# Kernel tuning notes

Hardware: AMD Instinct MI355X
Metric: run time of the kernel (lower is better)

## Reference

```python
import jax, jax.numpy as jnp
import numpy as np

N, T, IN_F, H, C_OUT, R = 50000, 128, 6, 32, 32, 16
NUM_EDGES, N_INC = 2000, 150000


def setup_inputs() -> dict:
    key = jax.random.key(0)
    ks = jax.random.split(key, 16)
    s = 0.1  # param scale
    return {
        "price_input": jax.random.normal(ks[0], (N, T, IN_F), jnp.float32),
        "concept": jax.random.normal(ks[1], (N_INC,), jnp.float32),
        "W_ih": jax.random.normal(ks[2], (3 * H, IN_F), jnp.float32) * s,
        "W_hh": jax.random.normal(ks[3], (3 * H, H), jnp.float32) * s,
        "b_ih": jax.random.normal(ks[4], (3 * H,), jnp.float32) * s,
        "b_hh": jax.random.normal(ks[5], (3 * H,), jnp.float32) * s,
        "W1": jax.random.normal(ks[6], (C_OUT, H), jnp.float32) * s,
        "b1": jax.random.normal(ks[7], (C_OUT,), jnp.float32) * s,
        "W2": jax.random.normal(ks[8], (H, C_OUT), jnp.float32) * s,
        "b2": jax.random.normal(ks[9], (H,), jnp.float32) * s,
        "Wl": jax.random.normal(ks[10], (R, H), jnp.float32) * s,
        "bl": jax.random.normal(ks[11], (R,), jnp.float32) * s,
        "node_idx": jax.random.randint(ks[12], (N_INC,), 0, N, dtype=jnp.int32),
        "edge_idx": jax.random.randint(ks[13], (N_INC,), 0, NUM_EDGES, dtype=jnp.int32),
    }


def gru_last_hidden(x, W_ih, W_hh, b_ih, b_hh):
    # x: [N, T, IN_F] -> final hidden state [N, H] (PyTorch GRU, gate order r,z,n)
    gi_all = jnp.einsum('nti,gi->tng', x, W_ih) + b_ih  # [T, N, 3H]
    h0 = jnp.zeros((x.shape[0], W_hh.shape[1]), x.dtype)

    def step(h, gi):
        gh = h @ W_hh.T + b_hh
        ir, iz, i_n = jnp.split(gi, 3, axis=-1)
        hr, hz, h_n = jnp.split(gh, 3, axis=-1)
        r = jax.nn.sigmoid(ir + hr)
        z = jax.nn.sigmoid(iz + hz)
        n = jnp.tanh(i_n + r * h_n)
        return (1.0 - z) * n + z * h, None

    hT, _ = jax.lax.scan(step, h0, gi_all)
    return hT


def hypergraph_conv(x, W, b, node_idx, edge_idx, num_nodes, num_edges):
    # PyG HypergraphConv, use_attention=False, hyperedge_weight=1:
    # out = D^{-1} H B^{-1} H^T (X W^T) + b
    xw = x @ W.T  # [N, F_out]
    ones = jnp.ones(node_idx.shape[0], x.dtype)
    B = jax.ops.segment_sum(ones, edge_idx, num_segments=num_edges)
    Binv = jnp.where(B > 0, 1.0 / B, 0.0)
    edge_feat = jax.ops.segment_sum(xw[node_idx], edge_idx, num_segments=num_edges)
    edge_feat = edge_feat * Binv[:, None]
    D = jax.ops.segment_sum(ones, node_idx, num_segments=num_nodes)
    Dinv = jnp.where(D > 0, 1.0 / D, 0.0)
    out = jax.ops.segment_sum(edge_feat[edge_idx], node_idx, num_segments=num_nodes)
    return out * Dinv[:, None] + b


def reference(price_input, concept, W_ih, W_hh, b_ih, b_hh, W1, b1, W2, b2, Wl, bl, node_idx, edge_idx):
    # concept is only consumed on the PreAttn path (disabled here), kept for signature parity.
    num_nodes = price_input.shape[0]
    output = gru_last_hidden(price_input, W_ih, W_hh, b_ih, b_hh)  # query[0] -> [N, c_in]
    output = jax.nn.leaky_relu(output, 0.01)
    x = jax.nn.leaky_relu(
        hypergraph_conv(output, W1, b1, node_idx, edge_idx, num_nodes, NUM_EDGES), 0.2)
    x = jax.nn.leaky_relu(
        hypergraph_conv(x, W2, b2, node_idx, edge_idx, num_nodes, NUM_EDGES), 0.2)
    return jax.nn.leaky_relu(x @ Wl.T + bl, 0.01)  # [N, len(rr_num)]
```

## Files before the change

### kernel.cpp

```cpp
#include <hip/hip_runtime.h>
#include <hip/hip_bf16.h>
#include <cstdint>

#define NN 50000
#define TT 128
#define INF 6
#define HH 32
#define NE 2000
#define NI 150000
#define RR 16

typedef __attribute__((ext_vector_type(4)))  float f32x4;
typedef __attribute__((ext_vector_type(16))) float f32x16;
typedef __attribute__((ext_vector_type(8)))  short short8;

__device__ __forceinline__ float lrelu(float x, float s){ return x > 0.f ? x : s*x; }

__device__ __forceinline__ unsigned pk2(float a, float b){
  union { __hip_bfloat162 h; unsigned u; } t;
  t.h = __float22bfloat162_rn(make_float2(a, b));
  return t.u;
}
__device__ __forceinline__ void pkhl(float a, float b, unsigned &hi, unsigned &lo){
  hi = pk2(a, b);
  float ha = __uint_as_float(hi << 16);
  float hb = __uint_as_float(hi & 0xFFFF0000u);
  lo = pk2(a - ha, b - hb);
}
__device__ __forceinline__ unsigned pksplit(float x){
  unsigned h = pk2(x, 0.f) & 0xFFFFu;
  float hf = __uint_as_float(h << 16);
  unsigned l = pk2(x - hf, 0.f) & 0xFFFFu;
  return h | (l << 16);
}
__device__ __forceinline__ short8 mk8(unsigned a, unsigned b, unsigned c, unsigned d){
  union { unsigned u[4]; short8 v; } t;
  t.u[0]=a; t.u[1]=b; t.u[2]=c; t.u[3]=d;
  return t.v;
}
#define MFMA32 __builtin_amdgcn_mfma_f32_32x32x16_bf16

__global__ __launch_bounds__(64,2) void gru_mfma(
    const float* __restrict__ price,
    const float* __restrict__ W_ih, const float* __restrict__ W_hh,
    const float* __restrict__ b_ih, const float* __restrict__ b_hh,
    const float* __restrict__ W1,
    float* __restrict__ xw, float* __restrict__ eaccZ)
{
  __shared__ __align__(16) unsigned xs[2][2048];

  const int lane = threadIdx.x;
  const int a    = lane & 31;
  const int hb   = lane >> 5;
  const int n0   = blockIdx.x*32;

  { int gt = blockIdx.x*64 + lane; if (gt < NE*HH) eaccZ[gt] = 0.f; }

  for (int idx = lane; idx < 512; idx += 64){
    int bsel = idx >> 8, rem = idx & 255;
    int nd = rem >> 3, t7 = rem & 7;
    int swz = (nd&7)<<2;
    xs[bsel][nd*64 + ((t7*8+6) ^ swz)] = 0x3F803F80u;
    xs[bsel][nd*64 + ((t7*8+7) ^ swz)] = 0u;
  }

  short8 AxA[3], Ahh[3][2], Ahl[3][2];
#pragma unroll
  for (int T=0; T<3; T++){
    const int gr = T*32 + a;
    const float sc = (T<2) ? -1.44269504f : 2.88539008f;
    const float* vi = W_ih + gr*INF;
    const float w0=vi[0]*sc, w1=vi[1]*sc, w2=vi[2]*sc, w3=vi[3]*sc, w4=vi[4]*sc, w5=vi[5]*sc;
    const float bias = (b_ih[gr] + ((T<2) ? b_hh[gr] : 0.f)) * sc;
    if (hb==0) AxA[T] = mk8(pk2(w0,w1), pk2(w2,w3), pk2(w4,w5), pk2(w0,w1));
    else       AxA[T] = mk8(pk2(w2,w3), pk2(w4,w5), pksplit(bias), 0u);
#pragma unroll
    for (int m=0; m<2; m++){
      const float* wp = W_hh + gr*HH + m*16 + hb*8;
      float4 wa = *(const float4*)(wp);
      float4 wb = *(const float4*)(wp+4);
      wa.x*=sc; wa.y*=sc; wa.z*=sc; wa.w*=sc;
      wb.x*=sc; wb.y*=sc; wb.z*=sc; wb.w*=sc;
      unsigned h0,l0,h1,l1,h2,l2,h3,l3;
      pkhl(wa.x,wa.y,h0,l0); pkhl(wa.z,wa.w,h1,l1);
      pkhl(wb.x,wb.y,h2,l2); pkhl(wb.z,wb.w,h3,l3);
      Ahh[T][m] = mk8(h0,h1,h2,h3);
      Ahl[T][m] = mk8(l0,l1,l2,l3);
    }
  }
  f32x16 BHN;
#pragma unroll
  for (int r=0; r<16; r++){
    int row = (r&3) + 8*(r>>2) + 4*hb;
    BHN[r] = b_hh[2*HH + row] * 2.88539008f;
  }
  const f32x16 Z16 = {0.f,0.f,0.f,0.f,0.f,0.f,0.f,0.f,0.f,0.f,0.f,0.f,0.f,0.f,0.f,0.f};

  float h[16];
#pragma unroll
  for (int r=0;r<16;r++) h[r]=0.f;
  short8 Bh1 = mk8(0,0,0,0), Bh2 = mk8(0,0,0,0);

  float4 ld[6];
#define PREFETCH(C) { \
  _Pragma("unroll") \
  for (int q=0;q<6;q++){ \
    int id=q*64+lane, a2=id/12, off=id%12; \
    int na=n0+a2; if (na>NN-1) na=NN-1; \
    ld[q] = *(const float4*)(price + (size_t)na*(TT*INF) + (C)*48 + off*4); \
  } }
#define STAGE(BUF) { \
  _Pragma("unroll") \
  for (int q=0;q<6;q++){ \
    int id=q*64+lane, a2=id/12, off=id%12; \
    int swz=(a2&7)<<2; unsigned* row=(BUF)+a2*64; \
    _Pragma("unroll") \
    for (int p=0;p<2;p++){ \
      float e0 = p? ld[q].z : ld[q].x; \
      float e1 = p? ld[q].w : ld[q].y; \
      int b = off*4 + p*2; int ttl = b/6; int ii = b - ttl*6; \
      unsigned hi_, lo_; pkhl(e0, e1, hi_, lo_); \
      row[(ttl*8 + (ii>>1)) ^ swz]     = hi_; \
      row[(ttl*8 + 3 + (ii>>1)) ^ swz] = lo_; \
    } } }

  PREFETCH(0); STAGE(&xs[0][0]);

  const int roff = (hb<<2) ^ ((a&7)<<2);

#pragma unroll 1
  for (int c=0;c<16;c++){
    if (c<15) PREFETCH(c+1);
    const unsigned* cell = &xs[c&1][a*64];
    unsigned* sb = &xs[(c&1)^1][0];
#pragma unroll 1
    for (int tt=0; tt<8; tt++){
      union{uint4 u; short8 s;} cv;
      cv.u = *(const uint4*)(cell + ((tt*8) ^ roff));
      f32x16 aR  = MFMA32(AxA[0], cv.s, Z16, 0,0,0);
      f32x16 aZ  = MFMA32(AxA[1], cv.s, Z16, 0,0,0);
      f32x16 aNX = MFMA32(AxA[2], cv.s, Z16, 0,0,0);
      f32x16 aNH = MFMA32(Ahh[2][0], Bh1, BHN, 0,0,0);
      aR = MFMA32(Ahh[0][0], Bh1, aR, 0,0,0); aR = MFMA32(Ahh[0][1], Bh2, aR, 0,0,0);
      aR = MFMA32(Ahl[0][0], Bh1, aR, 0,0,0); aR = MFMA32(Ahl[0][1], Bh2, aR, 0,0,0);
      aZ = MFMA32(Ahh[1][0], Bh1, aZ, 0,0,0); aZ = MFMA32(Ahh[1][1], Bh2, aZ, 0,0,0);
      aZ = MFMA32(Ahl[1][0], Bh1, aZ, 0,0,0); aZ = MFMA32(Ahl[1][1], Bh2, aZ, 0,0,0);
      aNH= MFMA32(Ahh[2][1], Bh2, aNH,0,0,0);
      aNH= MFMA32(Ahl[2][0], Bh1, aNH,0,0,0); aNH= MFMA32(Ahl[2][1], Bh2, aNH,0,0,0);
#define GUPD(hvar, AR, AZ, ANX, ANH) { \
      float er = __builtin_amdgcn_exp2f(AR); \
      float rr = __builtin_amdgcn_rcpf(1.f + er); \
      float p  = (ANX) + rr*(ANH); \
      float ez = __builtin_amdgcn_exp2f(AZ); \
      float et = __builtin_amdgcn_exp2f(p); \
      float etp = et + 1.f, etm = et - 1.f; \
      float num = hvar*etp + ez*etm; \
      float den = (1.f + ez) * etp; \
      hvar = num * __builtin_amdgcn_rcpf(den); }
#pragma unroll
      for (int r=0;r<16;r++) GUPD(h[r], aR[r], aZ[r], aNX[r], aNH[r]);
      unsigned c0=pk2(h[0],h[1]),  c1=pk2(h[2],h[3]),  c2=pk2(h[4],h[5]),  c3=pk2(h[6],h[7]);
      unsigned c4=pk2(h[8],h[9]),  c5=pk2(h[10],h[11]), c6=pk2(h[12],h[13]), c7=pk2(h[14],h[15]);
      unsigned p0=__shfl_xor(c0,32,64), p1=__shfl_xor(c1,32,64);
      unsigned p2=__shfl_xor(c2,32,64), p3=__shfl_xor(c3,32,64);
      unsigned p4=__shfl_xor(c4,32,64), p5=__shfl_xor(c5,32,64);
      unsigned p6=__shfl_xor(c6,32,64), p7=__shfl_xor(c7,32,64);
      unsigned v0 = hb? p2 : c0, v1 = hb? p3 : c1, v2 = hb? c2 : p0, v3 = hb? c3 : p1;
      unsigned w0 = hb? p6 : c4, w1 = hb? p7 : c5, w2 = hb? c6 : p4, w3 = hb? c7 : p5;
      Bh1 = mk8(v0,v1,v2,v3);
      Bh2 = mk8(w0,w1,w2,w3);
    }
    if (c<15) STAGE(sb);
  }

  float* ldsF = (float*)&xs[0][0];
#pragma unroll
  for (int r=0;r<16;r++){
    int row = (r&3) + 8*(r>>2) + 4*hb;
    ldsF[a*33 + row] = lrelu(h[r], 0.01f);
  }
  float b1v[8], b2v[8];
#pragma unroll
  for (int e=0;e<8;e++){
    b1v[e] = ldsF[a*33 + hb*8 + e];
    b2v[e] = ldsF[a*33 + 16 + hb*8 + e];
  }
  unsigned q0,s0,q1,s1,q2,s2,q3,s3;
  pkhl(b1v[0],b1v[1],q0,s0); pkhl(b1v[2],b1v[3],q1,s1);
  pkhl(b1v[4],b1v[5],q2,s2); pkhl(b1v[6],b1v[7],q3,s3);
  short8 Brh1 = mk8(q0,q1,q2,q3), Brl1 = mk8(s0,s1,s2,s3);
  pkhl(b2v[0],b2v[1],q0,s0); pkhl(b2v[2],b2v[3],q1,s1);
  pkhl(b2v[4],b2v[5],q2,s2); pkhl(b2v[6],b2v[7],q3,s3);
  short8 Brh2 = mk8(q0,q1,q2,q3), Brl2 = mk8(s0,s1,s2,s3);
  short8 W1h[2], W1l[2];
#pragma unroll
  for (int m=0;m<2;m++){
    const float* wp = W1 + a*HH + m*16 + hb*8;
    float4 wa = *(const float4*)(wp);
    float4 wb = *(const float4*)(wp+4);
    unsigned h0,l0,h1,l1,h2,l2,h3,l3;
    pkhl(wa.x,wa.y,h0,l0); pkhl(wa.z,wa.w,h1,l1);
    pkhl(wb.x,wb.y,h2,l2); pkhl(wb.z,wb.w,h3,l3);
    W1h[m] = mk8(h0,h1,h2,h3);
    W1l[m] = mk8(l0,l1,l2,l3);
  }
  f32x16 o = MFMA32(W1h[0], Brh1, Z16, 0,0,0);
  o = MFMA32(W1h[1], Brh2, o, 0,0,0);
  o = MFMA32(W1h[0], Brl1, o, 0,0,0);
  o = MFMA32(W1h[1], Brl2, o, 0,0,0);
  o = MFMA32(W1l[0], Brh1, o, 0,0,0);
  o = MFMA32(W1l[1], Brh2, o, 0,0,0);
#pragma unroll
  for (int r=0;r<16;r++){
    int row = (r&3) + 8*(r>>2) + 4*hb;
    ldsF[a*33 + row] = o[r];
  }
  {
    int nn = lane>>1, f0 = (lane&1)*16;
    if (n0 + nn < NN){
#pragma unroll
      for (int q=0;q<4;q++){
        float4 v;
        v.x = ldsF[nn*33 + f0 + q*4 + 0];
        v.y = ldsF[nn*33 + f0 + q*4 + 1];
        v.z = ldsF[nn*33 + f0 + q*4 + 2];
        v.w = ldsF[nn*33 + f0 + q*4 + 3];
        *(float4*)(xw + (size_t)(n0+nn)*HH + f0 + q*4) = v;
      }
    }
  }
}

template<bool COUNT>
__global__ __launch_bounds__(256) void scat_e(const float* __restrict__ xw, const int* __restrict__ nidx,
                                              const int* __restrict__ eidx, float* __restrict__ eacc,
                                              float* __restrict__ degD, float* __restrict__ degB){
  int idx = blockIdx.x*256 + threadIdx.x;
  int i = idx >> 5, f = idx & 31;
  int nd = nidx[i], e = eidx[i];
  if (COUNT && f == 0){
    atomicAdd(&degD[nd], 1.f);
    atomicAdd(&degB[e], 1.f);
  }
  atomicAdd(&eacc[(size_t)e*HH + f], xw[(size_t)nd*HH + f]);
}
template __global__ void scat_e<true>(const float*, const int*, const int*, float*, float*, float*);
template __global__ void scat_e<false>(const float*, const int*, const int*, float*, float*, float*);

__global__ __launch_bounds__(256) void scat_n(const float* __restrict__ eacc, const float* __restrict__ degB,
                                              const int* __restrict__ nidx, const int* __restrict__ eidx,
                                              float* __restrict__ nacc){
  int idx = blockIdx.x*256 + threadIdx.x;
  int i = idx >> 5, f = idx & 31;
  int nd = nidx[i], e = eidx[i];
  float b = degB[e];
  float binv = b > 0.f ? 1.f/b : 0.f;
  atomicAdd(&nacc[(size_t)nd*HH + f], eacc[(size_t)e*HH + f]*binv);
}

__global__ __launch_bounds__(256) void finmm(float* __restrict__ nacc, const float* __restrict__ degD,
                                             const float* __restrict__ bias, const float* __restrict__ W,
                                             float* __restrict__ Y, float* __restrict__ eacc){
  __shared__ float sWt[HH*HH];
  __shared__ float sX[8*HH];
  int tid = threadIdx.x;
  if (blockIdx.x < 250) eacc[blockIdx.x*256 + tid] = 0.f;
  int f0 = tid>>5, k = tid&31;
#pragma unroll
  for (int q=0;q<4;q++) sWt[k*HH + (q*8+f0)] = W[(q*8+f0)*HH + k];
  size_t base = (size_t)blockIdx.x*8*HH;
  int n = blockIdx.x*8 + (tid>>5);
  float d = degD[n];
  float dinv = d > 0.f ? 1.f/d : 0.f;
  sX[tid] = lrelu(nacc[base + tid]*dinv + bias[tid&31], 0.2f);
  nacc[base + tid] = 0.f;
  __syncthreads();
  float a = 0.f;
#pragma unroll
  for (int kk=0;kk<HH;kk++) a += sX[(tid>>5)*HH+kk]*sWt[kk*HH+(tid&31)];
  Y[base + tid] = a;
}

__global__ __launch_bounds__(256) void fin_final(const float* __restrict__ nacc, const float* __restrict__ degD,
                                                 const float* __restrict__ b2, const float* __restrict__ Wl,
                                                 const float* __restrict__ bl, float* __restrict__ out){
  __shared__ float sWl[HH*RR];
  __shared__ float sX[8*HH];
  int tid = threadIdx.x;
#pragma unroll
  for (int q=0;q<2;q++){
    int idx = q*256 + tid;
    int r = idx >> 5, kk = idx & 31;
    sWl[kk*RR + r] = Wl[idx];
  }
  size_t base = (size_t)blockIdx.x*8*HH;
  int n = blockIdx.x*8 + (tid>>5);
  float d = degD[n];
  float dinv = d > 0.f ? 1.f/d : 0.f;
  sX[tid] = lrelu(nacc[base + tid]*dinv + b2[tid&31], 0.2f);
  __syncthreads();
  int ln = tid>>5, r = tid&31;
  if (r < RR){
    float a = bl[r];
#pragma unroll
    for (int kk=0;kk<HH;kk++) a += sX[ln*HH+kk]*sWl[kk*RR+r];
    out[(size_t)(blockIdx.x*8+ln)*RR + r] = lrelu(a, 0.01f);
  }
}

extern "C" void kernel_launch(void* const* d_in, const int* in_sizes, int n_in,
                              void* d_out, int out_size, void* d_ws, size_t ws_size,
                              hipStream_t stream){
  const float* price = (const float*)d_in[0];
  const float* W_ih = (const float*)d_in[2];
  const float* W_hh = (const float*)d_in[3];
  const float* b_ih = (const float*)d_in[4];
  const float* b_hh = (const float*)d_in[5];
  const float* W1   = (const float*)d_in[6];
  const float* b1   = (const float*)d_in[7];
  const float* W2   = (const float*)d_in[8];
  const float* b2   = (const float*)d_in[9];
  const float* Wl   = (const float*)d_in[10];
  const float* bl   = (const float*)d_in[11];
  const int* nidx   = (const int*)d_in[12];
  const int* eidx   = (const int*)d_in[13];
  float* out = (float*)d_out;

  float* ws   = (float*)d_ws;
  float* xw   = ws;
  float* nacc = ws + 1600000;
  float* degD = ws + 3200000;
  float* degB = ws + 3250000;
  float* eacc = out;

  hipMemsetAsync(nacc, 0, (1600000+52000)*sizeof(float), stream);

  gru_mfma<<<1563, 64, 0, stream>>>(price, W_ih, W_hh, b_ih, b_hh, W1, xw, eacc);

  scat_e<true><<<18750, 256, 0, stream>>>(xw, nidx, eidx, eacc, degD, degB);
  scat_n<<<18750, 256, 0, stream>>>(eacc, degB, nidx, eidx, nacc);
  finmm<<<6250, 256, 0, stream>>>(nacc, degD, b1, W2, xw, eacc);

  scat_e<false><<<18750, 256, 0, stream>>>(xw, nidx, eidx, eacc, degD, degB);
  scat_n<<<18750, 256, 0, stream>>>(eacc, degB, nidx, eidx, nacc);
  fin_final<<<6250, 256, 0, stream>>>(nacc, degD, b2, Wl, bl, out);
}
```

Before: 347.3 us.

## Replace atomic edge scatter with CSR-sorted per-edge gather

Builds a CSR list of incident nodes per hyperedge on every call: count, scan, then fill. The edge aggregation then becomes one block per edge that sums its node features and applies the 1/B normalisation, with no atomics. This removes the heavily contended float atomics onto only 2000 edge rows. In exchange it adds three small preprocessing kernels and keeps CSR scratch inside the output buffer.

```diff
diff --git a/kernel.cpp b/kernel.cpp
--- a/kernel.cpp
+++ b/kernel.cpp
@@ -231,40 +231,80 @@
   }
 }
 
-template<bool COUNT>
-__global__ __launch_bounds__(256) void scat_e(const float* __restrict__ xw, const int* __restrict__ nidx,
-                                              const int* __restrict__ eidx, float* __restrict__ eacc,
-                                              float* __restrict__ degD, float* __restrict__ degB){
-  int idx = blockIdx.x*256 + threadIdx.x;
-  int i = idx >> 5, f = idx & 31;
-  int nd = nidx[i], e = eidx[i];
-  if (COUNT && f == 0){
-    atomicAdd(&degD[nd], 1.f);
-    atomicAdd(&degB[e], 1.f);
-  }
-  atomicAdd(&eacc[(size_t)e*HH + f], xw[(size_t)nd*HH + f]);
-}
-template __global__ void scat_e<true>(const float*, const int*, const int*, float*, float*, float*);
-template __global__ void scat_e<false>(const float*, const int*, const int*, float*, float*, float*);
-
-__global__ __launch_bounds__(256) void scat_n(const float* __restrict__ eacc, const float* __restrict__ degB,
+__global__ __launch_bounds__(256) void csr_count(const int* __restrict__ eidx, const int* __restrict__ nidx,
+                                                 int* __restrict__ ecnt, float* __restrict__ degD){
+  int i = blockIdx.x*256 + threadIdx.x;
+  if (i < NI){
+    atomicAdd(&ecnt[eidx[i]], 1);
+    atomicAdd(&degD[nidx[i]], 1.f);
+  }
+}
+
+__global__ __launch_bounds__(256) void escan(int* __restrict__ ecur, int* __restrict__ eoff){
+  __shared__ int wt[4];
+  int tid = threadIdx.x, lane = tid & 63, wv = tid >> 6;
+  int base = tid*8;
+  int c[8]; int s = 0;
+#pragma unroll
+  for (int k=0;k<8;k++){ int i=base+k; c[k] = (i<NE) ? ecur[i] : 0; s += c[k]; }
+  int inc = s;
+#pragma unroll
+  for (int o=1;o<64;o<<=1){ int v=__shfl_up(inc,o,64); if (lane>=o) inc += v; }
+  if (lane==63) wt[wv] = inc;
+  __syncthreads();
+  if (tid==0){ int r=0; for (int t=0;t<4;t++){ int v=wt[t]; wt[t]=r; r+=v; } }
+  __syncthreads();
+  int run = wt[wv] + inc - s;
+#pragma unroll
+  for (int k=0;k<8;k++){ int i=base+k; if (i<NE){ eoff[i]=run; ecur[i]=run; run += c[k]; } }
+  if (tid==0) eoff[NE] = NI;
+}
+
+__global__ __launch_bounds__(256) void csr_fill(const int* __restrict__ nidx, const int* __restrict__ eidx,
+                                                int* __restrict__ ecur, int* __restrict__ elist){
+  int i = blockIdx.x*256 + threadIdx.x;
+  if (i < NI){
+    int se = atomicAdd(&ecur[eidx[i]], 1);
+    elist[se] = nidx[i];
+  }
+}
+
+__global__ __launch_bounds__(256) void egather(const float* __restrict__ xw, const int* __restrict__ elist,
+                                               const int* __restrict__ eoff, float* __restrict__ eacc){
+  __shared__ float red[8][HH];
+  int e = blockIdx.x;
+  int tid = threadIdx.x;
+  int f = tid & 31, grp = tid >> 5;
+  int o0 = eoff[e], o1 = eoff[e+1];
+  float acc = 0.f;
+  for (int j = o0 + grp; j < o1; j += 8)
+    acc += xw[(size_t)elist[j]*HH + f];
+  red[grp][f] = acc;
+  __syncthreads();
+  if (tid < 32){
+    float s = red[0][f]+red[1][f]+red[2][f]+red[3][f]
+            + red[4][f]+red[5][f]+red[6][f]+red[7][f];
+    int d = o1 - o0;
+    float bi = d > 0 ? 1.f/(float)d : 0.f;
+    eacc[(size_t)e*HH + f] = s*bi;
+  }
+}
+
+__global__ __launch_bounds__(256) void scat_n(const float* __restrict__ eacc,
                                               const int* __restrict__ nidx, const int* __restrict__ eidx,
                                               float* __restrict__ nacc){
   int idx = blockIdx.x*256 + threadIdx.x;
   int i = idx >> 5, f = idx & 31;
   int nd = nidx[i], e = eidx[i];
-  float b = degB[e];
-  float binv = b > 0.f ? 1.f/b : 0.f;
-  atomicAdd(&nacc[(size_t)nd*HH + f], eacc[(size_t)e*HH + f]*binv);
+  atomicAdd(&nacc[(size_t)nd*HH + f], eacc[(size_t)e*HH + f]);
 }
 
 __global__ __launch_bounds__(256) void finmm(float* __restrict__ nacc, const float* __restrict__ degD,
                                              const float* __restrict__ bias, const float* __restrict__ W,
-                                             float* __restrict__ Y, float* __restrict__ eacc){
+                                             float* __restrict__ Y){
   __shared__ float sWt[HH*HH];
   __shared__ float sX[8*HH];
   int tid = threadIdx.x;
-  if (blockIdx.x < 250) eacc[blockIdx.x*256 + tid] = 0.f;
   int f0 = tid>>5, k = tid&31;
 #pragma unroll
   for (int q=0;q<4;q++) sWt[k*HH + (q*8+f0)] = W[(q*8+f0)*HH + k];
@@ -307,6 +347,11 @@
     out[(size_t)(blockIdx.x*8+ln)*RR + r] = lrelu(a, 0.01f);
   }
 }
+
+#define O_EACC  0
+#define O_EOFF  64000
+#define O_ECUR  66001
+#define O_ELIST 68001
 
 extern "C" void kernel_launch(void* const* d_in, const int* in_sizes, int n_in,
                               void* d_out, int out_size, void* d_ws, size_t ws_size,
@@ -325,23 +370,32 @@
   const int* nidx   = (const int*)d_in[12];
   const int* eidx   = (const int*)d_in[13];
   float* out = (float*)d_out;
+  int*  outI = (int*)d_out;
 
   float* ws   = (float*)d_ws;
   float* xw   = ws;
   float* nacc = ws + 1600000;
   float* degD = ws + 3200000;
-  float* degB = ws + 3250000;
-  float* eacc = out;
-
-  hipMemsetAsync(nacc, 0, (1600000+52000)*sizeof(float), stream);
+
+  float* eacc = out  + O_EACC;
+  int* eoff   = outI + O_EOFF;
+  int* ecur   = outI + O_ECUR;
+  int* elist  = outI + O_ELIST;
+
+  hipMemsetAsync(nacc, 0, (1600000+50000)*sizeof(float), stream);
+  hipMemsetAsync(ecur, 0, NE*sizeof(int), stream);
+
+  csr_count<<<586, 256, 0, stream>>>(eidx, nidx, ecur, degD);
+  escan<<<1, 256, 0, stream>>>(ecur, eoff);
+  csr_fill<<<586, 256, 0, stream>>>(nidx, eidx, ecur, elist);
 
   gru_mfma<<<1563, 64, 0, stream>>>(price, W_ih, W_hh, b_ih, b_hh, W1, xw, eacc);
 
-  scat_e<true><<<18750, 256, 0, stream>>>(xw, nidx, eidx, eacc, degD, degB);
-  scat_n<<<18750, 256, 0, stream>>>(eacc, degB, nidx, eidx, nacc);
-  finmm<<<6250, 256, 0, stream>>>(nacc, degD, b1, W2, xw, eacc);
-
-  scat_e<false><<<18750, 256, 0, stream>>>(xw, nidx, eidx, eacc, degD, degB);
-  scat_n<<<18750, 256, 0, stream>>>(eacc, degB, nidx, eidx, nacc);
+  egather<<<NE, 256, 0, stream>>>(xw, elist, eoff, eacc);
+  scat_n<<<18750, 256, 0, stream>>>(eacc, nidx, eidx, nacc);
+  finmm<<<6250, 256, 0, stream>>>(nacc, degD, b1, W2, xw);
+
+  egather<<<NE, 256, 0, stream>>>(xw, elist, eoff, eacc);
+  scat_n<<<18750, 256, 0, stream>>>(eacc, nidx, eidx, nacc);
   fin_final<<<6250, 256, 0, stream>>>(nacc, degD, b2, Wl, bl, out);
 }
```

Measured after the change: 353.7 us. No clear change (+1.8%).
